# Optimization experiments

Hardware: AMD Instinct MI355X
Metric: run time of the kernel (lower is better)

The kernel has to match this reference:

```python
import jax, jax.numpy as jnp
import numpy as np


def _conv(x, w, b, stride=1):
    # NCHW conv, 3x3 kernel, padding=1
    y = jax.lax.conv_general_dilated(
        x, w, (stride, stride), [(1, 1), (1, 1)],
        dimension_numbers=("NCHW", "OIHW", "NCHW"))
    return y + b[None, :, None, None]


def setup_inputs() -> dict:
    key = jax.random.key(0)
    ks = jax.random.split(key, 13)
    s = 0.05
    d = jnp.float32
    return {
        "x": jax.random.normal(ks[0], (1, 3, 512, 512), d),
        "low0_w": jax.random.normal(ks[1], (64, 3, 3, 3), d) * s,
        "low0_b": jax.random.normal(ks[2], (64,), d) * s,
        "ll_rh_w": jax.random.normal(ks[3], (4, 61, 61, 3, 3), d) * s,
        "ll_rh_b": jax.random.normal(ks[4], (4, 61), d) * s,
        "ll_lh_w": jax.random.normal(ks[5], (4, 3, 3, 3, 3), d) * s,
        "ll_lh_b": jax.random.normal(ks[6], (4, 3), d) * s,
        "hl0_w": jax.random.normal(ks[7], (64, 61, 3, 3), d) * s,
        "hl0_b": jax.random.normal(ks[8], (64,), d) * s,
        "hl_w": jax.random.normal(ks[9], (3, 64, 64, 3, 3), d) * s,
        "hl_b": jax.random.normal(ks[10], (3, 64), d) * s,
        "lin_w": jax.random.normal(ks[11], (30, 64), d) * s,
        "lin_b": jax.random.normal(ks[12], (30,), d) * s,
    }


def reference(x, low0_w, low0_b, ll_rh_w, ll_rh_b, ll_lh_w, ll_lh_b,
              hl0_w, hl0_b, hl_w, hl_b, lin_w, lin_b):
    # ---- low-level path: 64-channel full-resolution features ----
    I = _conv(x, low0_w, low0_b)  # (b,64,H,W)
    for i in range(ll_rh_w.shape[0]):
        rh = jax.nn.relu(_conv(I[:, :61], ll_rh_w[i], ll_rh_b[i]))
        lh = jnp.tanh(_conv(I[:, 61:], ll_lh_w[i], ll_lh_b[i]))
        I = jnp.concatenate([rh, lh], axis=1)
    # ---- high-level path: predicts 30 params -> 3x10 color transform ----
    h = _conv(I[:, :61], hl0_w, hl0_b)
    for i in range(hl_w.shape[0]):
        h = jax.nn.relu(_conv(h, hl_w[i], hl_b[i], stride=2))
        h = jax.lax.reduce_window(h, -jnp.inf, jax.lax.max,
                                  (1, 1, 2, 2), (1, 1, 2, 2), "VALID")
    g = h.mean(axis=(2, 3))            # (b,64) global average pool
    Wp = g @ lin_w.T + lin_b           # (b,30)
    Wm = Wp.reshape(3, 10)             # batch=1, matches torch reshape
    # ---- vectorized Tform: per-pixel quadratic feature expansion ----
    I3 = I[:, 61:]                     # (b,3,H,W)
    r, gc, bc = I3[:, 0], I3[:, 1], I3[:, 2]
    feats = jnp.stack([r * r, r * gc, r * bc, r,
                       gc * gc, gc * bc, gc,
                       bc * bc, bc, jnp.ones_like(r)], axis=1)  # (b,10,H,W)
    return jnp.einsum("ok,bkhw->bohw", Wm, feats)  # (b,3,H,W)
```

## Files before the change

### kernel.cpp

```cpp
#include <hip/hip_runtime.h>
#include <cstdint>

typedef _Float16 half8 __attribute__((ext_vector_type(8)));
typedef float f32x4 __attribute__((ext_vector_type(4)));

#define HW_ (512*512)

__global__ __launch_bounds__(256) void wtrans_k(
    const float* __restrict__ rh_w, const float* __restrict__ hl0_w,
    const float* __restrict__ hl_w, _Float16* __restrict__ wt,
    _Float16* __restrict__ zg)
{
    if (blockIdx.x == 0 && threadIdx.x < 32) zg[threadIdx.x] = (_Float16)0.f;
    int t = blockIdx.x * 256 + threadIdx.x;
    if (t >= 8 * 4608) return;
    int layer = t / 4608;
    int r = t - layer * 4608;
    int lane = r & 63, ci = r >> 6;
    int m = ci & 3, kk = (ci >> 2) & 1, s = ci >> 3;
    int o = m * 16 + (lane & 15);
    int cb = kk * 32 + ((lane >> 4) & 3) * 8;
    const float* w; int O, CIN;
    if (layer < 4)      { w = rh_w + (size_t)layer * 61 * 61 * 9; O = 61; CIN = 61; }
    else if (layer == 4){ w = hl0_w;                              O = 64; CIN = 61; }
    else                { w = hl_w + (size_t)(layer - 5) * 64 * 64 * 9; O = 64; CIN = 64; }
    half8 v;
    #pragma unroll
    for (int j = 0; j < 8; ++j) {
        int c = cb + j;
        float f = (o < O && c < CIN) ? w[((size_t)o * CIN + c) * 9 + s] : 0.f;
        v[j] = (_Float16)f;
    }
    *(half8*)(wt + (size_t)layer * 36864 + (size_t)r * 8) = v;
}

__global__ __launch_bounds__(256)
void low0_k(const float* __restrict__ x, const float* __restrict__ w,
            const float* __restrict__ bias, _Float16* __restrict__ M,
            float* __restrict__ L)
{
    __shared__ float tile[3 * 324];
    const int tx = threadIdx.x & 15, ty = threadIdx.x >> 4;
    const int bx = blockIdx.x, by = blockIdx.y, z = blockIdx.z;
    const int ox = bx * 16 + tx, oy = by * 16 + ty;
    const int ix0 = bx * 16 - 1, iy0 = by * 16 - 1;

    for (int i = threadIdx.x; i < 3 * 324; i += 256) {
        int c = i / 324, p = i - c * 324;
        int iy = p / 18, ix = p - iy * 18;
        int gy = iy0 + iy, gx = ix0 + ix;
        float v = 0.f;
        if ((unsigned)gy < 512u && (unsigned)gx < 512u)
            v = x[(size_t)c * HW_ + (size_t)gy * 512 + gx];
        tile[i] = v;
    }
    __syncthreads();

    float p9[3][9];
    #pragma unroll
    for (int c = 0; c < 3; ++c)
        #pragma unroll
        for (int dy = 0; dy < 3; ++dy)
            #pragma unroll
            for (int dx = 0; dx < 3; ++dx)
                p9[c][dy * 3 + dx] = tile[c * 324 + (ty + dy) * 18 + tx + dx];

    float acc[16];
    #pragma unroll
    for (int o = 0; o < 16; ++o) {
        int oc = z * 16 + o;
        float a = bias[oc];
        const float* wo = w + (size_t)oc * 27;
        #pragma unroll
        for (int c = 0; c < 3; ++c)
            #pragma unroll
            for (int k = 0; k < 9; ++k)
                a = fmaf(p9[c][k], wo[c * 9 + k], a);
        acc[o] = a;
    }

    const size_t pix = (size_t)oy * 512 + ox;
    half8 h0, h1;
    #pragma unroll
    for (int o = 0; o < 8; ++o) { h0[o] = (_Float16)acc[o]; h1[o] = (_Float16)acc[8 + o]; }
    _Float16* orow = M + pix * 64 + z * 16;
    *(half8*)(orow)     = h0;
    *(half8*)(orow + 8) = h1;
    if (z == 3) {
        #pragma unroll
        for (int o = 13; o < 16; ++o)
            L[(size_t)(o - 13) * HW_ + pix] = acc[o];
    }
}

template<int O, int ACT, int DOLH>
__global__ __launch_bounds__(256, 2)
void conv_mfma_k(const _Float16* __restrict__ in, const _Float16* __restrict__ wt,
                 const float* __restrict__ bias, _Float16* __restrict__ out,
                 const float* __restrict__ L_in, const float* __restrict__ lhw,
                 const float* __restrict__ lhb, float* __restrict__ L_out,
                 const _Float16* __restrict__ zg)
{
    __shared__ _Float16 __attribute__((aligned(16))) in_t[2592 * 8];
    __shared__ _Float16 __attribute__((aligned(16))) wbuf[2][4096];
    __shared__ float lh_t[DOLH ? 3 * 324 : 4];
    const int tid = threadIdx.x;
    const int l = tid & 63, wv = tid >> 6;
    const int px = l & 15, g = l >> 4;
    const int bx = blockIdx.x, by = blockIdx.y;
    const int iy0 = by * 16 - 1, ix0 = bx * 16 - 1;

    #pragma unroll
    for (int k = 0; k < 11; ++k) {
        int i = tid + (k << 8);
        if (i < 2592) {
            int p = i >> 3, jl = i & 7;
            int iy = p / 18, ix = p - iy * 18;
            int gy = iy0 + iy, gx = ix0 + ix;
            int j = jl ^ (p & 7);
            const _Float16* src = ((unsigned)gy < 512u && (unsigned)gx < 512u)
                ? in + ((size_t)gy * 512 + gx) * 64 + j * 8 : zg;
            __builtin_amdgcn_global_load_lds(
                (const __attribute__((address_space(1))) void*)src,
                (__attribute__((address_space(3))) void*)(in_t + (size_t)(i - l) * 8),
                16, 0, 0);
        }
    }
    #pragma unroll
    for (int it = 0; it < 2; ++it) {
        int ci = (it << 8) + tid;
        __builtin_amdgcn_global_load_lds(
            (const __attribute__((address_space(1))) void*)(wt + ci * 8),
            (__attribute__((address_space(3))) void*)(wbuf[0] + (size_t)(ci - l) * 8),
            16, 0, 0);
    }
    if (DOLH) {
        for (int i = tid; i < 3 * 324; i += 256) {
            int c = i / 324, p = i - c * 324;
            int iy = p / 18, ix = p - iy * 18;
            int gy = iy0 + iy, gx = ix0 + ix;
            float v = 0.f;
            if ((unsigned)gy < 512u && (unsigned)gx < 512u)
                v = L_in[(size_t)c * HW_ + (size_t)gy * 512 + gx];
            lh_t[i] = v;
        }
    }
    __syncthreads();

    float bs[4][4];
    #pragma unroll
    for (int m = 0; m < 4; ++m)
        #pragma unroll
        for (int r = 0; r < 4; ++r) {
            int o = m * 16 + g * 4 + r;
            bs[m][r] = (o < O) ? bias[o] : 0.f;
        }

    f32x4 acc[4][4];
    #pragma unroll
    for (int m = 0; m < 4; ++m)
        #pragma unroll
        for (int f = 0; f < 4; ++f) acc[m][f] = (f32x4){0.f, 0.f, 0.f, 0.f};

    #pragma unroll
    for (int s = 0; s < 9; ++s) {
        if (s < 8) {
            #pragma unroll
            for (int it = 0; it < 2; ++it) {
                int ci = (it << 8) + tid;
                __builtin_amdgcn_global_load_lds(
                    (const __attribute__((address_space(1))) void*)(wt + ((s + 1) << 12) + ci * 8),
                    (__attribute__((address_space(3))) void*)(wbuf[(s + 1) & 1] + (size_t)(ci - l) * 8),
                    16, 0, 0);
            }
        }
        const _Float16* wb = wbuf[s & 1];
        half8 a[8];
        #pragma unroll
        for (int q = 0; q < 8; ++q)
            a[q] = *(const half8*)(wb + (q << 9) + l * 8);

        const int dy = s / 3, dx = s - dy * 3;
        #pragma unroll
        for (int f = 0; f < 4; ++f) {
            int ipix = (4 * wv + f + dy) * 18 + px + dx;
            int rb = ipix * 64, sw = (ipix & 7) << 3;
            #pragma unroll
            for (int kk = 0; kk < 2; ++kk) {
                half8 b = *(const half8*)&in_t[rb + ((kk * 32 + g * 8) ^ sw)];
                #pragma unroll
                for (int m = 0; m < 4; ++m)
                    acc[m][f] = __builtin_amdgcn_mfma_f32_16x16x32_f16(
                        a[kk * 4 + m], b, acc[m][f], 0, 0, 0);
            }
        }
        __syncthreads();
    }

    if (DOLH) {
        const int tx = tid & 15, ty = tid >> 4;
        const size_t pix = (size_t)(by * 16 + ty) * 512 + bx * 16 + tx;
        #pragma unroll
        for (int oc = 0; oc < 3; ++oc) {
            float a = lhb[oc];
            #pragma unroll
            for (int c = 0; c < 3; ++c)
                #pragma unroll
                for (int t9 = 0; t9 < 9; ++t9) {
                    int dy = t9 / 3, dx = t9 - dy * 3;
                    a = fmaf(lh_t[c * 324 + (ty + dy) * 18 + tx + dx],
                             lhw[(oc * 3 + c) * 9 + t9], a);
                }
            L_out[(size_t)oc * HW_ + pix] = tanhf(a);
        }
    }

    #pragma unroll
    for (int f = 0; f < 4; ++f) {
        const int p = (4 * wv + f) * 16 + px;
        const int sw = p & 7;
        #pragma unroll
        for (int m = 0; m < 4; ++m) {
            union { _Float16 h[4]; uint2 u; } pk;
            #pragma unroll
            for (int r = 0; r < 4; ++r) {
                int o = m * 16 + g * 4 + r;
                float v = acc[m][f][r] + bs[m][r];
                if (ACT) v = fmaxf(v, 0.f);
                pk.h[r] = (o < O) ? (_Float16)v : (_Float16)0.f;
            }
            int chunk = (m * 2 + (g >> 1)) ^ sw;
            *(uint2*)&in_t[p * 64 + chunk * 8 + (g & 1) * 4] = pk.u;
        }
    }
    __syncthreads();
    #pragma unroll
    for (int k = 0; k < 8; ++k) {
        int q = (k << 8) + tid;
        int p = q >> 3, jc = q & 7;
        half8 v = *(const half8*)&in_t[p * 64 + ((jc ^ (p & 7)) * 8)];
        int row = p >> 4, col = p & 15;
        _Float16* dst = out + (((size_t)(by * 16 + row) * 512) + bx * 16 + col) * 64 + jc * 8;
        *(half8*)dst = v;
    }
}

template<int FP32OUT>
__global__ __launch_bounds__(256, 3)
void conv_s2_pool_k(const _Float16* __restrict__ in, int Hin,
                    const _Float16* __restrict__ wt,
                    const float* __restrict__ bias, void* __restrict__ outv,
                    const _Float16* __restrict__ zg)
{
    const int Hp = Hin >> 2;
    __shared__ _Float16 __attribute__((aligned(16))) in_t[2312 * 8];
    __shared__ _Float16 __attribute__((aligned(16))) wbuf[2][4096];
    const int tid = threadIdx.x;
    const int l = tid & 63, wv = tid >> 6;
    const int n = l & 15, g = l >> 4;
    const int bx = blockIdx.x, by = blockIdx.y;
    const int iy0 = by * 16 - 1, ix0 = bx * 16 - 1;

    #pragma unroll
    for (int k = 0; k < 10; ++k) {
        int i = tid + (k << 8);
        if (i < 2312) {
            int p = i >> 3, jl = i & 7;
            int iy = p / 17, ix = p - iy * 17;
            int gy = iy0 + iy, gx = ix0 + ix;
            int j = jl ^ (p & 7);
            const _Float16* src =
                ((unsigned)gy < (unsigned)Hin && (unsigned)gx < (unsigned)Hin)
                    ? in + ((size_t)gy * Hin + gx) * 64 + j * 8 : zg;
            __builtin_amdgcn_global_load_lds(
                (const __attribute__((address_space(1))) void*)src,
                (__attribute__((address_space(3))) void*)(in_t + (size_t)(i - l) * 8),
                16, 0, 0);
        }
    }
    #pragma unroll
    for (int it = 0; it < 2; ++it) {
        int ci = (it << 8) + tid;
        __builtin_amdgcn_global_load_lds(
            (const __attribute__((address_space(1))) void*)(wt + ci * 8),
            (__attribute__((address_space(3))) void*)(wbuf[0] + (size_t)(ci - l) * 8),
            16, 0, 0);
    }
    __syncthreads();

    float bs[4];
    #pragma unroll
    for (int r = 0; r < 4; ++r) bs[r] = bias[wv * 16 + g * 4 + r];

    f32x4 acc[4];
    #pragma unroll
    for (int f = 0; f < 4; ++f) acc[f] = (f32x4){0.f, 0.f, 0.f, 0.f};

    const int py_lo = n >> 3, pxc = n & 7;
    #pragma unroll
    for (int s = 0; s < 9; ++s) {
        if (s < 8) {
            #pragma unroll
            for (int it = 0; it < 2; ++it) {
                int ci = (it << 8) + tid;
                __builtin_amdgcn_global_load_lds(
                    (const __attribute__((address_space(1))) void*)(wt + ((s + 1) << 12) + ci * 8),
                    (__attribute__((address_space(3))) void*)(wbuf[(s + 1) & 1] + (size_t)(ci - l) * 8),
                    16, 0, 0);
            }
        }
        const _Float16* wb = wbuf[s & 1];
        half8 a[2];
        #pragma unroll
        for (int kk = 0; kk < 2; ++kk)
            a[kk] = *(const half8*)(wb + ((kk * 4 + wv) << 9) + l * 8);

        const int dy = s / 3, dx = s - dy * 3;
        #pragma unroll
        for (int f = 0; f < 4; ++f) {
            int py = 2 * f + py_lo;
            int ipix = (2 * py + dy) * 17 + 2 * pxc + dx;
            int rb = ipix * 64, sw = (ipix & 7) << 3;
            #pragma unroll
            for (int kk = 0; kk < 2; ++kk) {
                half8 b = *(const half8*)&in_t[rb + ((kk * 32 + g * 8) ^ sw)];
                acc[f] = __builtin_amdgcn_mfma_f32_16x16x32_f16(a[kk], b, acc[f], 0, 0, 0);
            }
        }
        __syncthreads();
    }

    #pragma unroll
    for (int f = 0; f < 4; ++f)
        #pragma unroll
        for (int r = 0; r < 4; ++r) {
            float v = fmaxf(acc[f][r] + bs[r], 0.f);
            v = fmaxf(v, __shfl_xor(v, 1));
            v = fmaxf(v, __shfl_xor(v, 8));
            if ((l & 9) == 0) {
                int o = wv * 16 + g * 4 + r;
                size_t pp = ((size_t)(by * 4 + f) * Hp + bx * 4 + (n >> 1)) * 64 + o;
                if (FP32OUT) ((float*)outv)[pp] = v;
                else         ((_Float16*)outv)[pp] = (_Float16)v;
            }
        }
}

__global__ void meanlin_k(const float* __restrict__ h,
                          const float* __restrict__ lw,
                          const float* __restrict__ lb,
                          float* __restrict__ wm)
{
    __shared__ float g[64];
    int t = threadIdx.x;
    if (t < 64) {
        float s = 0.f;
        for (int p = 0; p < 64; ++p) s += h[p * 64 + t];
        g[t] = s * (1.f / 64.f);
    }
    __syncthreads();
    if (t < 30) {
        float s = lb[t];
        for (int c = 0; c < 64; ++c) s = fmaf(g[c], lw[t * 64 + c], s);
        wm[t] = s;
    }
}

__global__ __launch_bounds__(256)
void final_k(const float* __restrict__ I3, const float* __restrict__ wm,
             float* __restrict__ out)
{
    __shared__ float W[30];
    if (threadIdx.x < 30) W[threadIdx.x] = wm[threadIdx.x];
    __syncthreads();
    const int HW = 512 * 512;
    for (int i = blockIdx.x * blockDim.x + threadIdx.x; i < HW;
         i += gridDim.x * blockDim.x) {
        float r = I3[i], g = I3[HW + i], b = I3[2 * HW + i];
        float f[10] = { r * r, r * g, r * b, r, g * g, g * b, g, b * b, b, 1.f };
        #pragma unroll
        for (int o = 0; o < 3; ++o) {
            float s = 0.f;
            #pragma unroll
            for (int k = 0; k < 10; ++k) s = fmaf(W[o * 10 + k], f[k], s);
            out[(size_t)o * HW + i] = s;
        }
    }
}

extern "C" void kernel_launch(void* const* d_in, const int* in_sizes, int n_in,
                              void* d_out, int out_size, void* d_ws, size_t ws_size,
                              hipStream_t stream)
{
    const float* x      = (const float*)d_in[0];
    const float* low0_w = (const float*)d_in[1];
    const float* low0_b = (const float*)d_in[2];
    const float* rh_w   = (const float*)d_in[3];
    const float* rh_b   = (const float*)d_in[4];
    const float* lh_w   = (const float*)d_in[5];
    const float* lh_b   = (const float*)d_in[6];
    const float* hl0_w  = (const float*)d_in[7];
    const float* hl0_b  = (const float*)d_in[8];
    const float* hl_w   = (const float*)d_in[9];
    const float* hl_b   = (const float*)d_in[10];
    const float* lin_w  = (const float*)d_in[11];
    const float* lin_b  = (const float*)d_in[12];
    float* out = (float*)d_out;

    const size_t HW = 512 * 512;
    _Float16* M0 = (_Float16*)d_ws;
    _Float16* M1 = M0 + (size_t)64 * HW;
    _Float16* P0 = M1 + (size_t)64 * HW;
    _Float16* P1 = P0 + (size_t)16384 * 64;
    _Float16* WT = P1 + (size_t)1024 * 64;
    _Float16* ZG = WT + (size_t)8 * 36864;
    float*    P2 = (float*)(ZG + 32);
    float*    L0 = P2 + 64 * 64;
    float*    L1 = L0 + (size_t)3 * HW;
    float*    WM = L1 + (size_t)3 * HW;

    dim3 blk(256);
    dim3 g512(32, 32, 1);

    wtrans_k<<<dim3(144), blk, 0, stream>>>(rh_w, hl0_w, hl_w, WT, ZG);

    low0_k<<<dim3(32, 32, 4), blk, 0, stream>>>(x, low0_w, low0_b, M0, L0);

    _Float16* cur = M0; _Float16* nxt = M1;
    float* Lc = L0; float* Ln = L1;
    for (int i = 0; i < 4; ++i) {
        conv_mfma_k<61, 1, 1><<<g512, blk, 0, stream>>>(
            cur, WT + (size_t)i * 36864, rh_b + i * 61, nxt,
            Lc, lh_w + (size_t)i * 81, lh_b + i * 3, Ln, ZG);
        _Float16* t = cur; cur = nxt; nxt = t;
        float* tl = Lc; Lc = Ln; Ln = tl;
    }

    conv_mfma_k<64, 0, 0><<<g512, blk, 0, stream>>>(
        cur, WT + (size_t)4 * 36864, hl0_b, nxt,
        nullptr, nullptr, nullptr, nullptr, ZG);

    conv_s2_pool_k<0><<<dim3(32, 32), blk, 0, stream>>>(
        nxt, 512, WT + (size_t)5 * 36864, hl_b, (void*)P0, ZG);
    conv_s2_pool_k<0><<<dim3(8, 8), blk, 0, stream>>>(
        P0, 128, WT + (size_t)6 * 36864, hl_b + 64, (void*)P1, ZG);
    conv_s2_pool_k<1><<<dim3(2, 2), blk, 0, stream>>>(
        P1, 32, WT + (size_t)7 * 36864, hl_b + 128, (void*)P2, ZG);

    meanlin_k<<<dim3(1), dim3(64), 0, stream>>>(P2, lin_w, lin_b, WM);

    final_k<<<dim3(2048), blk, 0, stream>>>(Lc, WM, out);
}
```

Measured before the change: 228.9 us.

## Remap block IDs for XCD-local tiles and move tanh branch to epilogue

Launches the conv kernels on a 1D grid and remaps block IDs so that consecutive tiles handled by the same XCD (blockIdx mod 8) are spatially contiguous. This is meant to improve L2 reuse of halo rows across neighbouring tiles. It also removes the shared-memory staging of the 3-channel tanh branch. That branch is now computed at the end of the kernel from direct global loads held in registers, which cuts LDS use and one prologue loop but adds register pressure and redundant global reads.

New measurement: 217.5 us. -5.0%, faster.

```diff
diff --git a/kernel.cpp b/kernel.cpp
--- a/kernel.cpp
+++ b/kernel.cpp
@@ -103,11 +103,12 @@
 {
     __shared__ _Float16 __attribute__((aligned(16))) in_t[2592 * 8];
     __shared__ _Float16 __attribute__((aligned(16))) wbuf[2][4096];
-    __shared__ float lh_t[DOLH ? 3 * 324 : 4];
     const int tid = threadIdx.x;
     const int l = tid & 63, wv = tid >> 6;
     const int px = l & 15, g = l >> 4;
-    const int bx = blockIdx.x, by = blockIdx.y;
+    const int orig = blockIdx.x;
+    const int id = ((orig & 7) << 7) + (orig >> 3);
+    const int bx = id & 31, by = id >> 5;
     const int iy0 = by * 16 - 1, ix0 = bx * 16 - 1;
 
     #pragma unroll
@@ -134,17 +135,6 @@
             (__attribute__((address_space(3))) void*)(wbuf[0] + (size_t)(ci - l) * 8),
             16, 0, 0);
     }
-    if (DOLH) {
-        for (int i = tid; i < 3 * 324; i += 256) {
-            int c = i / 324, p = i - c * 324;
-            int iy = p / 18, ix = p - iy * 18;
-            int gy = iy0 + iy, gx = ix0 + ix;
-            float v = 0.f;
-            if ((unsigned)gy < 512u && (unsigned)gx < 512u)
-                v = L_in[(size_t)c * HW_ + (size_t)gy * 512 + gx];
-            lh_t[i] = v;
-        }
-    }
     __syncthreads();
 
     float bs[4][4];
@@ -195,24 +185,6 @@
             }
         }
         __syncthreads();
-    }
-
-    if (DOLH) {
-        const int tx = tid & 15, ty = tid >> 4;
-        const size_t pix = (size_t)(by * 16 + ty) * 512 + bx * 16 + tx;
-        #pragma unroll
-        for (int oc = 0; oc < 3; ++oc) {
-            float a = lhb[oc];
-            #pragma unroll
-            for (int c = 0; c < 3; ++c)
-                #pragma unroll
-                for (int t9 = 0; t9 < 9; ++t9) {
-                    int dy = t9 / 3, dx = t9 - dy * 3;
-                    a = fmaf(lh_t[c * 324 + (ty + dy) * 18 + tx + dx],
-                             lhw[(oc * 3 + c) * 9 + t9], a);
-                }
-            L_out[(size_t)oc * HW_ + pix] = tanhf(a);
-        }
     }
 
     #pragma unroll
@@ -243,9 +215,32 @@
         _Float16* dst = out + (((size_t)(by * 16 + row) * 512) + bx * 16 + col) * 64 + jc * 8;
         *(half8*)dst = v;
     }
-}
-
-template<int FP32OUT>
+
+    if (DOLH) {
+        const int tx = tid & 15, ty = tid >> 4;
+        const int oy = by * 16 + ty, ox = bx * 16 + tx;
+        float pv[27];
+        #pragma unroll
+        for (int c = 0; c < 3; ++c)
+            #pragma unroll
+            for (int d2 = 0; d2 < 9; ++d2) {
+                int gy = oy + d2 / 3 - 1, gx = ox + d2 % 3 - 1;
+                pv[c * 9 + d2] = ((unsigned)gy < 512u && (unsigned)gx < 512u)
+                    ? L_in[(size_t)c * HW_ + (size_t)gy * 512 + gx] : 0.f;
+            }
+        const size_t pix = (size_t)oy * 512 + ox;
+        #pragma unroll
+        for (int oc = 0; oc < 3; ++oc) {
+            float a = lhb[oc];
+            #pragma unroll
+            for (int k = 0; k < 27; ++k)
+                a = fmaf(pv[k], lhw[oc * 27 + k], a);
+            L_out[(size_t)oc * HW_ + pix] = tanhf(a);
+        }
+    }
+}
+
+template<int FP32OUT, int NB>
 __global__ __launch_bounds__(256, 3)
 void conv_s2_pool_k(const _Float16* __restrict__ in, int Hin,
                     const _Float16* __restrict__ wt,
@@ -258,7 +253,9 @@
     const int tid = threadIdx.x;
     const int l = tid & 63, wv = tid >> 6;
     const int n = l & 15, g = l >> 4;
-    const int bx = blockIdx.x, by = blockIdx.y;
+    int id = blockIdx.x;
+    if (NB == 32) id = ((id & 7) << 7) + (id >> 3);
+    const int bx = id % NB, by = id / NB;
     const int iy0 = by * 16 - 1, ix0 = bx * 16 - 1;
 
     #pragma unroll
@@ -420,7 +417,6 @@
     float*    WM = L1 + (size_t)3 * HW;
 
     dim3 blk(256);
-    dim3 g512(32, 32, 1);
 
     wtrans_k<<<dim3(144), blk, 0, stream>>>(rh_w, hl0_w, hl_w, WT, ZG);
 
@@ -429,22 +425,22 @@
     _Float16* cur = M0; _Float16* nxt = M1;
     float* Lc = L0; float* Ln = L1;
     for (int i = 0; i < 4; ++i) {
-        conv_mfma_k<61, 1, 1><<<g512, blk, 0, stream>>>(
+        conv_mfma_k<61, 1, 1><<<dim3(1024), blk, 0, stream>>>(
             cur, WT + (size_t)i * 36864, rh_b + i * 61, nxt,
             Lc, lh_w + (size_t)i * 81, lh_b + i * 3, Ln, ZG);
         _Float16* t = cur; cur = nxt; nxt = t;
         float* tl = Lc; Lc = Ln; Ln = tl;
     }
 
-    conv_mfma_k<64, 0, 0><<<g512, blk, 0, stream>>>(
+    conv_mfma_k<64, 0, 0><<<dim3(1024), blk, 0, stream>>>(
         cur, WT + (size_t)4 * 36864, hl0_b, nxt,
         nullptr, nullptr, nullptr, nullptr, ZG);
 
-    conv_s2_pool_k<0><<<dim3(32, 32), blk, 0, stream>>>(
+    conv_s2_pool_k<0, 32><<<dim3(1024), blk, 0, stream>>>(
         nxt, 512, WT + (size_t)5 * 36864, hl_b, (void*)P0, ZG);
-    conv_s2_pool_k<0><<<dim3(8, 8), blk, 0, stream>>>(
+    conv_s2_pool_k<0, 8><<<dim3(64), blk, 0, stream>>>(
         P0, 128, WT + (size_t)6 * 36864, hl_b + 64, (void*)P1, ZG);
-    conv_s2_pool_k<1><<<dim3(2, 2), blk, 0, stream>>>(
+    conv_s2_pool_k<1, 2><<<dim3(4), blk, 0, stream>>>(
         P1, 32, WT + (size_t)7 * 36864, hl_b + 128, (void*)P2, ZG);
 
     meanlin_k<<<dim3(1), dim3(64), 0, stream>>>(P2, lin_w, lin_b, WM);
```
